# Performance work log

Hardware: AMD Instinct MI355X
Metric: run time of the kernel (lower is better)

Reference implementation:

```python
import jax, jax.numpy as jnp
import numpy as np

B, N, T, NIN, NEMB, NH = 8, 512, 64, 64, 128, 128


def _sym_normalize(A):
    # D^{-1/2} A D^{-1/2}, degree = row sum; zero-safe
    d = jnp.sum(A, axis=-1)
    dinv = jnp.where(d > 0, 1.0 / jnp.sqrt(jnp.where(d > 0, d, 1.0)), 0.0)
    return A * dinv[..., :, None] * dinv[..., None, :]


def setup_inputs() -> dict:
    key = jax.random.key(0)
    ks = jax.random.split(key, 32)
    def lin(i, fan_in, fan_out):
        s = 1.0 / np.sqrt(fan_in)
        W = jax.random.uniform(ks[2 * i], (fan_in, fan_out), jnp.float32, -s, s)
        b = jax.random.uniform(ks[2 * i + 1], (fan_out,), jnp.float32, -s, s)
        return W, b
    Wse, bse = lin(0, NIN, NEMB)
    Wpe, bpe = lin(1, NH, NEMB)
    Wii, bii = lin(2, 2 * NEMB, NH)
    Whi, bhi = lin(3, NH, NH)
    Wif, bif = lin(4, 2 * NEMB, NH)
    Whf, bhf = lin(5, NH, NH)
    Wig, big = lin(6, 2 * NEMB, NH)
    Whg, bhg = lin(7, NH, NH)
    Wio, bio = lin(8, 2 * NEMB, NH)
    Who, bho = lin(9, NH, NH)
    Wout, bout = lin(10, NH, NIN)
    X = jax.random.normal(ks[22], (B, N, T, NIN), jnp.float32)
    A = jax.random.uniform(ks[23], (B, N, N), jnp.float32)
    return dict(X=X, A=A, Wse=Wse, bse=bse, Wpe=Wpe, bpe=bpe,
                Wii=Wii, bii=bii, Whi=Whi, bhi=bhi,
                Wif=Wif, bif=bif, Whf=Whf, bhf=bhf,
                Wig=Wig, big=big, Whg=Whg, bhg=bhg,
                Wio=Wio, bio=bio, Who=Who, bho=bho,
                Wout=Wout, bout=bout)


def reference(X, A, Wse, bse, Wpe, bpe, Wii, bii, Whi, bhi, Wif, bif,
              Whf, bhf, Wig, big, Whg, bhg, Wio, bio, Who, bho, Wout, bout):
    An = _sym_normalize(A)  # [B,N,N]
    X0 = X[:, :, 0, :]                       # [B,N,NIN]
    es = X0 @ Wse + bse                      # [B,N,NEMB], constant across steps
    h0 = jnp.zeros((X.shape[0], X.shape[1], NH), X.dtype)
    c0 = jnp.zeros_like(h0)

    def step(carry, _):
        Xi, c, h = carry
        H = jnp.einsum('bnm,bmh->bnh', An, h)    # graph pooling
        eh = H @ Wpe + bpe
        x = jnp.concatenate([es, eh], axis=-1)   # [B,N,2*NEMB]
        i_t = jax.nn.sigmoid(x @ Wii + bii + h @ Whi + bhi)
        f_t = jax.nn.sigmoid(x @ Wif + bif + h @ Whf + bhf)
        g_t = jnp.tanh(x @ Wig + big + h @ Whg + bhg)
        o_t = jax.nn.sigmoid(x @ Wio + bio + h @ Who + bho)
        c_t = f_t * c + i_t * g_t
        h_t = o_t * jnp.tanh(c_t)
        Xi_new = Xi + h_t @ Wout + bout
        return (Xi_new, c_t, h_t), Xi_new

    num_steps = X.shape[2] - 1
    _, Xs = jax.lax.scan(step, (X0, c0, h0), None, length=num_steps)  # [T-1,B,N,NIN]
    X_hat = jnp.concatenate([X0[None], Xs], axis=0)                   # [T,B,N,NIN]
    return jnp.transpose(X_hat, (1, 2, 0, 3))                         # [B,N,T,NIN]
```

## Files before the change

### kernel.cpp

```cpp
#include <hip/hip_runtime.h>
#include <math.h>

#define B_ 8
#define N_ 512
#define T_ 64
#define NIN_ 64
#define NE_ 128
#define NH_ 128
#define NR_ 4096

typedef __attribute__((ext_vector_type(8))) short s8_t;
typedef __attribute__((ext_vector_type(4))) short s4_t;
typedef __attribute__((ext_vector_type(4))) float f4_t;
typedef __attribute__((ext_vector_type(4))) int i4_t;
typedef __attribute__((ext_vector_type(2))) int i2_t;

__device__ __forceinline__ float sigm(float x) {
  x = fminf(fmaxf(x, -30.f), 30.f);
  return 1.f / (1.f + __expf(-x));
}
__device__ __forceinline__ float tanh_fast(float x) {
  x = fminf(fmaxf(x, -15.f), 15.f);
  float e = __expf(2.f * x);
  return (e - 1.f) / (e + 1.f);
}
__device__ __forceinline__ unsigned short f2b(float f) {
  union { float f; unsigned u; } v; v.f = f;
  unsigned r = (v.u + 0x7FFFu + ((v.u >> 16) & 1u)) >> 16;
  return (unsigned short)r;
}

__device__ __forceinline__ i4_t load_coherent16(const void* p) {
  i4_t r;
  asm volatile("global_load_dwordx4 %0, %1, off sc0 sc1"
               : "=v"(r) : "v"(p) : "memory");
  return r;
}
__device__ __forceinline__ void store_coherent8(void* p, i2_t v) {
  asm volatile("global_store_dwordx2 %0, %1, off sc0 sc1"
               :: "v"(p), "v"(v) : "memory");
}
__device__ __forceinline__ void wait_vm0() {
  asm volatile("s_waitcnt vmcnt(0)" ::: "memory");
}

__global__ __launch_bounds__(256) void k_setup1(
    const float* __restrict__ A,
    const float* __restrict__ bii, const float* __restrict__ bif,
    const float* __restrict__ big, const float* __restrict__ bio,
    const float* __restrict__ bhi, const float* __restrict__ bhf,
    const float* __restrict__ bhg, const float* __restrict__ bho,
    const float* __restrict__ bpe,
    const float* __restrict__ Wii, const float* __restrict__ Wif,
    const float* __restrict__ Wig, const float* __restrict__ Wio,
    const float* __restrict__ Wse, const float* __restrict__ Wout,
    float* __restrict__ dinv, float* __restrict__ bcat,
    unsigned short* __restrict__ WseP, unsigned short* __restrict__ WxeP,
    unsigned short* __restrict__ WoutP, int* __restrict__ cnt) {
  const int blk = blockIdx.x, t = threadIdx.x;
  if (blk < 1024) {
    int row = blk * 4 + (t >> 6);
    int lane = t & 63;
    const float* a = A + (size_t)row * N_;
    float s = 0.f;
    for (int j = lane; j < N_; j += 64) s += a[j];
    #pragma unroll
    for (int off = 32; off > 0; off >>= 1) s += __shfl_down(s, off);
    if (lane == 0) dinv[row] = (s > 0.f) ? rsqrtf(s) : 0.f;
  } else if (blk < 1026) {
    int col = (blk - 1024) * 256 + t;
    int g = col >> 7, j = col & 127;
    const float* bx = (g == 0) ? bii : (g == 1) ? bif : (g == 2) ? big : bio;
    const float* bh = (g == 0) ? bhi : (g == 1) ? bhf : (g == 2) ? bhg : bho;
    const float* Wx = (g == 0) ? Wii : (g == 1) ? Wif : (g == 2) ? Wig : Wio;
    float s = bx[j] + bh[j];
    for (int k = 0; k < NE_; k++) s += bpe[k] * Wx[(size_t)(128 + k) * NH_ + j];
    bcat[col] = s;
  } else if (blk < 1346) {
    int idx = (blk - 1026) * 256 + t;
    if (idx < 8192) {
      int k = idx >> 7, c = idx & 127;
      WseP[((size_t)(k >> 3) * 128 + c) * 8 + (k & 7)] = f2b(Wse[(size_t)k * 128 + c]);
    } else if (idx < 8192 + 65536) {
      int i = idx - 8192;
      int k = i >> 9, col = i & 511, g = col >> 7, j = col & 127;
      const float* Wx = (g == 0) ? Wii : (g == 1) ? Wif : (g == 2) ? Wig : Wio;
      WxeP[((size_t)(k >> 3) * 512 + col) * 8 + (k & 7)] = f2b(Wx[(size_t)k * 128 + j]);
    } else if (idx < 8192 + 65536 + 8192) {
      int i = idx - 8192 - 65536;
      int k = i >> 6, c = i & 63;
      WoutP[((size_t)(k >> 3) * 64 + c) * 8 + (k & 7)] = f2b(Wout[(size_t)k * 64 + c]);
    }
  } else {
    if (t < 128) cnt[t] = 0;
  }
}

__global__ __launch_bounds__(256) void k_setup2(
    const float* __restrict__ Wpe,
    const float* __restrict__ Whi, const float* __restrict__ Whf,
    const float* __restrict__ Whg, const float* __restrict__ Who,
    const float* __restrict__ Wii, const float* __restrict__ Wif,
    const float* __restrict__ Wig, const float* __restrict__ Wio,
    unsigned short* __restrict__ WUP2) {
  int idx = blockIdx.x * 256 + threadIdx.x;
  int k = idx >> 9, col = idx & 511, g = col >> 7, j = col & 127;
  float v;
  if (k < 128) {
    const float* Wx = (g == 0) ? Wii : (g == 1) ? Wif : (g == 2) ? Wig : Wio;
    float s = 0.f;
    for (int mm = 0; mm < 128; mm++)
      s += Wpe[(size_t)k * 128 + mm] * Wx[(size_t)(128 + mm) * 128 + j];
    v = s;
  } else {
    const float* Wh = (g == 0) ? Whi : (g == 1) ? Whf : (g == 2) ? Whg : Who;
    v = Wh[(size_t)(k - 128) * 128 + j];
  }
  WUP2[((size_t)(k >> 3) * 512 + col) * 8 + (k & 7)] = f2b(v);
}

__global__ __launch_bounds__(512, 2) void k_persist(
    const float* __restrict__ A, const float* __restrict__ dinv,
    const float* __restrict__ X,
    const unsigned short* __restrict__ WseP, const float* __restrict__ bse,
    const unsigned short* __restrict__ WxeP, const float* __restrict__ bcat,
    const unsigned short* __restrict__ WUP2,
    const unsigned short* __restrict__ WoutP, const float* __restrict__ bout,
    unsigned short* __restrict__ hP,
    int* __restrict__ cnt,
    float* __restrict__ out) {
  __shared__ __align__(16) unsigned short as[16][520];
  __shared__ __align__(16) unsigned short xh[16][264];
  __shared__ __align__(16) float ps[1536];

  const int t = threadIdx.x;
  const int b = blockIdx.x & 7;
  const int rt = blockIdx.x >> 3;
  const int r0 = b * N_ + rt * 16;
  const int l = t & 63, w = t >> 6, m = l & 15, kg = l >> 4;
  const int c = w * 16 + m;

  float* X0s = ps;
  float* dvb = ps + 1024;

  if (t < 512) dvb[t] = dinv[b * 512 + t];
  for (int i = t; i < 1024; i += 512) {
    int r = i >> 6, cc = i & 63;
    float v = X[((size_t)(r0 + r) * T_) * NIN_ + cc];
    X0s[i] = v;
    out[((size_t)(r0 + r) * T_) * NIN_ + cc] = v;
  }
  __syncthreads();
  for (int i = t; i < 1024; i += 512) xh[i >> 6][i & 63] = f2b(X0s[i]);
  for (int i = t; i < 8192; i += 512) {
    int r = i >> 9, k = i & 511;
    as[r][k] = f2b(A[(size_t)(r0 + r) * 512 + k] * dinv[r0 + r] * dvb[k]);
  }
  __syncthreads();
  {
    f4_t e;
    float bv = bse[c];
    #pragma unroll
    for (int r = 0; r < 4; r++) e[r] = bv;
    #pragma unroll
    for (int kc = 0; kc < 2; kc++) {
      s8_t a = *(const s8_t*)&xh[m][kc * 32 + kg * 8];
      s8_t bf = *(const s8_t*)&WseP[((size_t)(kc * 4 + kg) * 128 + c) * 8];
      e = __builtin_amdgcn_mfma_f32_16x16x32_bf16(a, bf, e, 0, 0, 0);
    }
    #pragma unroll
    for (int r = 0; r < 4; r++)
      xh[kg * 4 + r][128 + c] = f2b(e[r]);
  }
  __syncthreads();
  f4_t esr[4];
  #pragma unroll
  for (int g = 0; g < 4; g++) {
    float bv = bcat[g * 128 + c];
    #pragma unroll
    for (int r = 0; r < 4; r++) esr[g][r] = bv;
  }
  #pragma unroll
  for (int kc = 0; kc < 4; kc++) {
    s8_t a = *(const s8_t*)&xh[m][128 + kc * 32 + kg * 8];
    #pragma unroll
    for (int g = 0; g < 4; g++) {
      s8_t bf = *(const s8_t*)&WxeP[((size_t)(kc * 4 + kg) * 512 + g * 128 + c) * 8];
      esr[g] = __builtin_amdgcn_mfma_f32_16x16x32_bf16(a, bf, esr[g], 0, 0, 0);
    }
  }
  f4_t oacc = {0.f, 0.f, 0.f, 0.f};
  float bo = 0.f;
  if (w < 4) {
    bo = bout[w * 16 + m];
    #pragma unroll
    for (int r = 0; r < 4; r++) oacc[r] = X0s[(kg * 4 + r) * 64 + w * 16 + m];
  }
  float cs[4] = {0.f, 0.f, 0.f, 0.f};
  s8_t wz[8][4];
  #pragma unroll
  for (int kc = 0; kc < 8; kc++)
    #pragma unroll
    for (int g = 0; g < 4; g++)
      wz[kc][g] = *(const s8_t*)&WUP2[((size_t)(kc * 4 + kg) * 512 + g * 128 + c) * 8];
  __syncthreads();
  for (int i = t; i < 16 * 264; i += 512) ((unsigned short*)xh)[i] = 0;
  __syncthreads();

  for (int tt = 1; tt < T_; tt++) {
    if (tt > 1) {
      const int need = 32 * (tt - 1);
      while (__hip_atomic_load(cnt + b * 16, __ATOMIC_RELAXED,
                               __HIP_MEMORY_SCOPE_SYSTEM) < need)
        __builtin_amdgcn_s_sleep(1);
      const unsigned short* hPb =
          hP + ((size_t)((tt - 1) & 1) * 8 + b) * 65536;
      i4_t hf[16];
      #pragma unroll
      for (int kc = 0; kc < 16; kc++)
        hf[kc] = load_coherent16(&hPb[((size_t)(kc * 4 + kg) * 128 + c) * 8]);
      f4_t ga = {0.f, 0.f, 0.f, 0.f};
      asm volatile("s_waitcnt vmcnt(8)"
                   : "+v"(hf[0]), "+v"(hf[1]), "+v"(hf[2]), "+v"(hf[3]),
                     "+v"(hf[4]), "+v"(hf[5]), "+v"(hf[6]), "+v"(hf[7])
                   :: "memory");
      #pragma unroll
      for (int kc = 0; kc < 8; kc++) {
        s8_t a = *(const s8_t*)&as[m][kc * 32 + kg * 8];
        ga = __builtin_amdgcn_mfma_f32_16x16x32_bf16(a, *(const s8_t*)&hf[kc],
                                                     ga, 0, 0, 0);
      }
      asm volatile("s_waitcnt vmcnt(0)"
                   : "+v"(hf[8]), "+v"(hf[9]), "+v"(hf[10]), "+v"(hf[11]),
                     "+v"(hf[12]), "+v"(hf[13]), "+v"(hf[14]), "+v"(hf[15])
                   :: "memory");
      #pragma unroll
      for (int kc = 8; kc < 16; kc++) {
        s8_t a = *(const s8_t*)&as[m][kc * 32 + kg * 8];
        ga = __builtin_amdgcn_mfma_f32_16x16x32_bf16(a, *(const s8_t*)&hf[kc],
                                                     ga, 0, 0, 0);
      }
      #pragma unroll
      for (int r = 0; r < 4; r++)
        xh[kg * 4 + r][c] = f2b(ga[r]);
      __syncthreads();
    }
    f4_t acc[4];
    #pragma unroll
    for (int g = 0; g < 4; g++) acc[g] = esr[g];
    #pragma unroll
    for (int kc = 0; kc < 8; kc++) {
      s8_t a = *(const s8_t*)&xh[m][kc * 32 + kg * 8];
      #pragma unroll
      for (int g = 0; g < 4; g++)
        acc[g] = __builtin_amdgcn_mfma_f32_16x16x32_bf16(a, wz[kc][g], acc[g], 0, 0, 0);
    }
    union { unsigned short u[4]; i2_t v; } hb;
    #pragma unroll
    for (int r = 0; r < 4; r++) {
      float it = sigm(acc[0][r]), ft = sigm(acc[1][r]);
      float gt = tanh_fast(acc[2][r]), ot = sigm(acc[3][r]);
      cs[r] = ft * cs[r] + it * gt;
      hb.u[r] = f2b(ot * tanh_fast(cs[r]));
    }
    if (tt < T_ - 1) {
      unsigned short* dst = hP + ((size_t)(tt & 1) * 8 + b) * 65536 +
                            (size_t)(rt * 2 + (kg >> 1)) * 1024 +
                            (size_t)c * 8 + (kg & 1) * 4;
      store_coherent8(dst, hb.v);
    }
    __syncthreads();
    #pragma unroll
    for (int r = 0; r < 4; r++)
      xh[kg * 4 + r][128 + c] = hb.u[r];
    if (tt < T_ - 1) wait_vm0();
    __syncthreads();
    if (tt < T_ - 1 && t == 0)
      __hip_atomic_fetch_add(cnt + b * 16, 1, __ATOMIC_RELAXED,
                             __HIP_MEMORY_SCOPE_SYSTEM);
    if (w < 4) {
      f4_t o = {0.f, 0.f, 0.f, 0.f};
      #pragma unroll
      for (int kc = 0; kc < 4; kc++) {
        s8_t a = *(const s8_t*)&xh[m][128 + kc * 32 + kg * 8];
        s8_t bf = *(const s8_t*)&WoutP[((size_t)(kc * 4 + kg) * 64 + w * 16 + m) * 8];
        o = __builtin_amdgcn_mfma_f32_16x16x32_bf16(a, bf, o, 0, 0, 0);
      }
      #pragma unroll
      for (int r = 0; r < 4; r++) {
        oacc[r] += o[r] + bo;
        out[((size_t)(r0 + kg * 4 + r) * T_ + tt) * NIN_ + w * 16 + m] = oacc[r];
      }
    }
  }
}

extern "C" void kernel_launch(void* const* d_in, const int* in_sizes, int n_in,
                              void* d_out, int out_size, void* d_ws, size_t ws_size,
                              hipStream_t stream) {
  const float* X    = (const float*)d_in[0];
  const float* A    = (const float*)d_in[1];
  const float* Wse  = (const float*)d_in[2];
  const float* bse  = (const float*)d_in[3];
  const float* Wpe  = (const float*)d_in[4];
  const float* bpe  = (const float*)d_in[5];
  const float* Wii  = (const float*)d_in[6];
  const float* bii  = (const float*)d_in[7];
  const float* Whi  = (const float*)d_in[8];
  const float* bhi  = (const float*)d_in[9];
  const float* Wif  = (const float*)d_in[10];
  const float* bif_ = (const float*)d_in[11];
  const float* Whf  = (const float*)d_in[12];
  const float* bhf  = (const float*)d_in[13];
  const float* Wig  = (const float*)d_in[14];
  const float* big_ = (const float*)d_in[15];
  const float* Whg  = (const float*)d_in[16];
  const float* bhg  = (const float*)d_in[17];
  const float* Wio  = (const float*)d_in[18];
  const float* bio  = (const float*)d_in[19];
  const float* Who  = (const float*)d_in[20];
  const float* bho  = (const float*)d_in[21];
  const float* Wout = (const float*)d_in[22];
  const float* bout = (const float*)d_in[23];
  float* out = (float*)d_out;
  char* ws = (char*)d_ws;

  size_t off = 0;
  float* dinv = (float*)(ws + off);                    off += 4096 * 4;
  float* bcat = (float*)(ws + off);                    off += 512 * 4;
  unsigned short* WUP2  = (unsigned short*)(ws + off); off += 131072 * 2;
  unsigned short* WseP  = (unsigned short*)(ws + off); off += 8192 * 2;
  unsigned short* WxeP  = (unsigned short*)(ws + off); off += 65536 * 2;
  unsigned short* WoutP = (unsigned short*)(ws + off); off += 8192 * 2;
  unsigned short* hP    = (unsigned short*)(ws + off); off += (size_t)2 * 8 * 65536 * 2;
  int* cnt = (int*)(ws + off);                         off += 128 * 4;

  k_setup1<<<1347, 256, 0, stream>>>(A, bii, bif_, big_, bio, bhi, bhf, bhg,
                                     bho, bpe, Wii, Wif, Wig, Wio, Wse, Wout,
                                     dinv, bcat, WseP, WxeP, WoutP, cnt);
  k_setup2<<<512, 256, 0, stream>>>(Wpe, Whi, Whf, Whg, Who,
                                    Wii, Wif, Wig, Wio, WUP2);

  void* args[] = {(void*)&A, (void*)&dinv, (void*)&X,
                  (void*)&WseP, (void*)&bse, (void*)&WxeP, (void*)&bcat,
                  (void*)&WUP2, (void*)&WoutP, (void*)&bout,
                  (void*)&hP, (void*)&cnt, (void*)&out};
  if (hipLaunchCooperativeKernel((const void*)k_persist, dim3(256), dim3(512),
                                 args, 0, stream) != hipSuccess) {
    k_persist<<<256, 512, 0, stream>>>(A, dinv, X, WseP, bse, WxeP, bcat,
                                       WUP2, WoutP, bout, hP, cnt, out);
  }
}
```

Baseline: 597.5 us.

## Use per-step fresh h buffers with plain loads and single-thread spin wait

Result: faster. 539.8 us (-9.7%).

```diff
diff --git a/kernel.cpp b/kernel.cpp
--- a/kernel.cpp
+++ b/kernel.cpp
@@ -128,9 +128,9 @@
     const unsigned short* __restrict__ WoutP, const float* __restrict__ bout,
     unsigned short* __restrict__ hP,
     int* __restrict__ cnt,
-    float* __restrict__ out) {
+    float* __restrict__ out, int fresh) {
   __shared__ __align__(16) unsigned short as[16][520];
-  __shared__ __align__(16) unsigned short xh[16][264];
+  __shared__ __align__(16) unsigned short xh[16][392];
   __shared__ __align__(16) float ps[1536];
 
   const int t = threadIdx.x;
@@ -204,42 +204,44 @@
     for (int g = 0; g < 4; g++)
       wz[kc][g] = *(const s8_t*)&WUP2[((size_t)(kc * 4 + kg) * 512 + g * 128 + c) * 8];
   __syncthreads();
-  for (int i = t; i < 16 * 264; i += 512) ((unsigned short*)xh)[i] = 0;
+  for (int i = t; i < 16 * 256; i += 512) {
+    int r = i >> 8, cc = i & 255;
+    xh[r][cc] = 0;
+  }
   __syncthreads();
 
   for (int tt = 1; tt < T_; tt++) {
+    const int hoff_old = 128 + ((tt - 1) & 1) * 128;
+    const int hoff_new = 128 + (tt & 1) * 128;
     if (tt > 1) {
-      const int need = 32 * (tt - 1);
-      while (__hip_atomic_load(cnt + b * 16, __ATOMIC_RELAXED,
-                               __HIP_MEMORY_SCOPE_SYSTEM) < need)
-        __builtin_amdgcn_s_sleep(1);
-      const unsigned short* hPb =
-          hP + ((size_t)((tt - 1) & 1) * 8 + b) * 65536;
+      if (t == 511) {
+        const int need = 32 * (tt - 1);
+        while (__hip_atomic_load(cnt + b * 16, __ATOMIC_RELAXED,
+                                 __HIP_MEMORY_SCOPE_SYSTEM) < need)
+          __builtin_amdgcn_s_sleep(4);
+      }
+      __syncthreads();
+      asm volatile("" ::: "memory");
+      const int bi = fresh ? (tt - 2) : ((tt - 1) & 1);
+      const unsigned short* hPb = hP + ((size_t)bi * 8 + b) * 65536;
       i4_t hf[16];
-      #pragma unroll
-      for (int kc = 0; kc < 16; kc++)
-        hf[kc] = load_coherent16(&hPb[((size_t)(kc * 4 + kg) * 128 + c) * 8]);
+      if (fresh) {
+        #pragma unroll
+        for (int kc = 0; kc < 16; kc++)
+          hf[kc] = *(const i4_t*)&hPb[((size_t)(kc * 4 + kg) * 128 + c) * 8];
+      } else {
+        #pragma unroll
+        for (int kc = 0; kc < 16; kc++)
+          hf[kc] = load_coherent16(&hPb[((size_t)(kc * 4 + kg) * 128 + c) * 8]);
+        wait_vm0();
+      }
       f4_t ga = {0.f, 0.f, 0.f, 0.f};
-      asm volatile("s_waitcnt vmcnt(8)"
-                   : "+v"(hf[0]), "+v"(hf[1]), "+v"(hf[2]), "+v"(hf[3]),
-                     "+v"(hf[4]), "+v"(hf[5]), "+v"(hf[6]), "+v"(hf[7])
-                   :: "memory");
-      #pragma unroll
-      for (int kc = 0; kc < 8; kc++) {
+      #pragma unroll
+      for (int kc = 0; kc < 16; kc++) {
         s8_t a = *(const s8_t*)&as[m][kc * 32 + kg * 8];
         ga = __builtin_amdgcn_mfma_f32_16x16x32_bf16(a, *(const s8_t*)&hf[kc],
                                                      ga, 0, 0, 0);
       }
-      asm volatile("s_waitcnt vmcnt(0)"
-                   : "+v"(hf[8]), "+v"(hf[9]), "+v"(hf[10]), "+v"(hf[11]),
-                     "+v"(hf[12]), "+v"(hf[13]), "+v"(hf[14]), "+v"(hf[15])
-                   :: "memory");
-      #pragma unroll
-      for (int kc = 8; kc < 16; kc++) {
-        s8_t a = *(const s8_t*)&as[m][kc * 32 + kg * 8];
-        ga = __builtin_amdgcn_mfma_f32_16x16x32_bf16(a, *(const s8_t*)&hf[kc],
-                                                     ga, 0, 0, 0);
-      }
       #pragma unroll
       for (int r = 0; r < 4; r++)
         xh[kg * 4 + r][c] = f2b(ga[r]);
@@ -250,7 +252,8 @@
     for (int g = 0; g < 4; g++) acc[g] = esr[g];
     #pragma unroll
     for (int kc = 0; kc < 8; kc++) {
-      s8_t a = *(const s8_t*)&xh[m][kc * 32 + kg * 8];
+      const int koff = (kc < 4) ? kc * 32 : hoff_old + (kc - 4) * 32;
+      s8_t a = *(const s8_t*)&xh[m][koff + kg * 8];
       #pragma unroll
       for (int g = 0; g < 4; g++)
         acc[g] = __builtin_amdgcn_mfma_f32_16x16x32_bf16(a, wz[kc][g], acc[g], 0, 0, 0);
@@ -263,17 +266,17 @@
       cs[r] = ft * cs[r] + it * gt;
       hb.u[r] = f2b(ot * tanh_fast(cs[r]));
     }
+    #pragma unroll
+    for (int r = 0; r < 4; r++)
+      xh[kg * 4 + r][hoff_new + c] = hb.u[r];
     if (tt < T_ - 1) {
-      unsigned short* dst = hP + ((size_t)(tt & 1) * 8 + b) * 65536 +
+      const int bo_ = fresh ? (tt - 1) : (tt & 1);
+      unsigned short* dst = hP + ((size_t)bo_ * 8 + b) * 65536 +
                             (size_t)(rt * 2 + (kg >> 1)) * 1024 +
                             (size_t)c * 8 + (kg & 1) * 4;
       store_coherent8(dst, hb.v);
-    }
-    __syncthreads();
-    #pragma unroll
-    for (int r = 0; r < 4; r++)
-      xh[kg * 4 + r][128 + c] = hb.u[r];
-    if (tt < T_ - 1) wait_vm0();
+      wait_vm0();
+    }
     __syncthreads();
     if (tt < T_ - 1 && t == 0)
       __hip_atomic_fetch_add(cnt + b * 16, 1, __ATOMIC_RELAXED,
@@ -282,7 +285,7 @@
       f4_t o = {0.f, 0.f, 0.f, 0.f};
       #pragma unroll
       for (int kc = 0; kc < 4; kc++) {
-        s8_t a = *(const s8_t*)&xh[m][128 + kc * 32 + kg * 8];
+        s8_t a = *(const s8_t*)&xh[m][hoff_new + kc * 32 + kg * 8];
         s8_t bf = *(const s8_t*)&WoutP[((size_t)(kc * 4 + kg) * 64 + w * 16 + m) * 8];
         o = __builtin_amdgcn_mfma_f32_16x16x32_bf16(a, bf, o, 0, 0, 0);
       }
@@ -332,8 +335,10 @@
   unsigned short* WseP  = (unsigned short*)(ws + off); off += 8192 * 2;
   unsigned short* WxeP  = (unsigned short*)(ws + off); off += 65536 * 2;
   unsigned short* WoutP = (unsigned short*)(ws + off); off += 8192 * 2;
-  unsigned short* hP    = (unsigned short*)(ws + off); off += (size_t)2 * 8 * 65536 * 2;
   int* cnt = (int*)(ws + off);                         off += 128 * 4;
+  unsigned short* hP    = (unsigned short*)(ws + off);
+  const size_t fresh_bytes = (size_t)62 * 8 * 65536 * 2;
+  int fresh = (ws_size >= off + fresh_bytes) ? 1 : 0;
 
   k_setup1<<<1347, 256, 0, stream>>>(A, bii, bif_, big_, bio, bhi, bhf, bhg,
                                      bho, bpe, Wii, Wif, Wig, Wio, Wse, Wout,
@@ -344,10 +349,10 @@
   void* args[] = {(void*)&A, (void*)&dinv, (void*)&X,
                   (void*)&WseP, (void*)&bse, (void*)&WxeP, (void*)&bcat,
                   (void*)&WUP2, (void*)&WoutP, (void*)&bout,
-                  (void*)&hP, (void*)&cnt, (void*)&out};
+                  (void*)&hP, (void*)&cnt, (void*)&out, (void*)&fresh};
   if (hipLaunchCooperativeKernel((const void*)k_persist, dim3(256), dim3(512),
                                  args, 0, stream) != hipSuccess) {
     k_persist<<<256, 512, 0, stream>>>(A, dinv, X, WseP, bse, WxeP, bcat,
-                                       WUP2, WoutP, bout, hP, cnt, out);
-  }
-}
+                                       WUP2, WoutP, bout, hP, cnt, out, fresh);
+  }
+}
```
